# Kernel tuning notes

Measured on AMD Instinct MI355X. Metric: run time of the kernel, lower is better.

Reference implementation:

```python
import jax, jax.numpy as jnp
import numpy as np

# fixed seed frame used by rotate_matrix (same as torch init_matrix)
INIT_MATRIX = jnp.array([[-np.sqrt(0.5), np.sqrt(1.5), 0.0],
                         [-np.sqrt(2.0), 0.0, 0.0],
                         [0.0, 0.0, 0.0]], dtype=jnp.float32)

N_ATOMS = 3_000_000  # 1M residues * 3 backbone atoms
FN = 3000            # number of fragments; L = N_ATOMS // FN = 1000


def setup_inputs() -> dict:
    key = jax.random.key(0)
    k1, k2, k3 = jax.random.split(key, 3)
    # realistic internal coordinates: bond lengths ~1.33-1.53A, angles ~1.9-2.1 rad,
    # dihedrals uniform in [-pi, pi]
    bond_length = 1.33 + 0.2 * jax.random.uniform(k1, (N_ATOMS,), dtype=jnp.float32)
    bond_angle = 1.9 + 0.2 * jax.random.uniform(k2, (N_ATOMS,), dtype=jnp.float32)
    dhd = (2.0 * jax.random.uniform(k3, (N_ATOMS,), dtype=jnp.float32) - 1.0) * np.float32(np.pi)
    inner_tensor = jnp.stack([bond_length, bond_angle, dhd], axis=1)  # [N,3]
    # non-collinear initial frame (first 3 mainchain atoms)
    mainchain_coord_tensor = jnp.array([[0.0, 0.0, 0.0],
                                        [1.46, 0.0, 0.0],
                                        [2.0, 1.4, 0.0]], dtype=jnp.float32)
    return {"inner_tensor": inner_tensor, "fn": FN,
            "mainchain_coord_tensor": mainchain_coord_tensor}


def _frame_rows(A, B, C):
    # rows [bc, cross(n,bc), n]; torch builds M = rows^T and does M @ p,
    # which equals p @ rows
    bc = C - B
    bc = bc / jnp.linalg.norm(bc)
    n = jnp.cross(B - A, bc)
    n = n / jnp.linalg.norm(n)
    return jnp.stack([bc, jnp.cross(n, bc), n])  # [3,3]


def _extend_fragment(local_pts):
    # sequential NeRF extension in the fragment-local frame (rotate_matrix)
    def step(carry, p):
        A, B, C = carry
        D = p @ _frame_rows(A, B, C) + C
        return (B, C, D), D
    init = (INIT_MATRIX[0], INIT_MATRIX[1], INIT_MATRIX[2])
    _, pts = jax.lax.scan(step, init, local_pts)
    return pts  # [L,3]


def reference(inner_tensor, fn, mainchain_coord_tensor):
    N = inner_tensor.shape[0]
    L = N // fn
    bond_length = inner_tensor[:, 0]
    bond_angle = inner_tensor[:, 1]
    dhd = inner_tensor[:, 2]
    # psi/omiga/phy re-interleave (identity permutation when N % 3 == 0)
    dhd_v = jnp.stack([dhd[0::3], dhd[1::3], dhd[2::3]], axis=1).reshape(N)
    r_cos = bond_length * jnp.cos(bond_angle)
    r_sin = bond_length * jnp.sin(bond_angle)
    point = jnp.stack([r_cos, jnp.cos(dhd_v) * r_sin, jnp.sin(dhd_v) * r_sin], axis=1)  # [N,3]
    # independent local fragment builds (vmapped over fragments)
    local = jax.vmap(_extend_fragment)(point.reshape(fn, L, 3))  # [fn,L,3]
    frame0 = mainchain_coord_tensor[:3]
    # sequential placement of fragments into global frame (srf2f)
    def place(frame, loc):
        A, B, C = frame[0], frame[1], frame[2]
        g = loc @ _frame_rows(A, B, C) + C  # [L,3]
        return g[-3:], g
    _, glob = jax.lax.scan(place, frame0, local)  # [fn,L,3]
    return jnp.concatenate([frame0, glob.reshape(fn * L, 3)], axis=0)  # [3+N,3]
```

## Files before the change

kernel.cpp:

```cpp
#include <hip/hip_runtime.h>

#define NSTEPS 25
#define SUBF   (NSTEPS * 3)
#define BLK    256

struct Xf { float m[12]; };

__device__ __forceinline__ Xf xf_identity() {
    Xf o;
    o.m[0]=1.f;o.m[1]=0.f;o.m[2]=0.f;
    o.m[3]=0.f;o.m[4]=1.f;o.m[5]=0.f;
    o.m[6]=0.f;o.m[7]=0.f;o.m[8]=1.f;
    o.m[9]=0.f;o.m[10]=0.f;o.m[11]=0.f;
    return o;
}

__device__ __forceinline__ Xf xf_compose(const Xf& a, const Xf& b) {
    Xf o;
#pragma unroll
    for (int i = 0; i < 3; ++i)
#pragma unroll
        for (int c = 0; c < 3; ++c)
            o.m[i*3+c] = b.m[i*3+0]*a.m[0+c] + b.m[i*3+1]*a.m[3+c] + b.m[i*3+2]*a.m[6+c];
#pragma unroll
    for (int c = 0; c < 3; ++c)
        o.m[9+c] = b.m[9+0]*a.m[0+c] + b.m[9+1]*a.m[3+c] + b.m[9+2]*a.m[6+c] + a.m[9+c];
    return o;
}

__device__ __forceinline__ void xf_store_g(float* p, const Xf& x) {
    float4* q = (float4*)p;
    q[0] = make_float4(x.m[0], x.m[1], x.m[2],  x.m[3]);
    q[1] = make_float4(x.m[4], x.m[5], x.m[6],  x.m[7]);
    q[2] = make_float4(x.m[8], x.m[9], x.m[10], x.m[11]);
}

__device__ __forceinline__ Xf xf_load_g(const float* p) {
    const float4* q = (const float4*)p;
    float4 a = q[0], b = q[1], c = q[2];
    Xf o;
    o.m[0]=a.x; o.m[1]=a.y; o.m[2]=a.z;  o.m[3]=a.w;
    o.m[4]=b.x; o.m[5]=b.y; o.m[6]=b.z;  o.m[7]=b.w;
    o.m[8]=c.x; o.m[9]=c.y; o.m[10]=c.z; o.m[11]=c.w;
    return o;
}

__device__ __forceinline__ Xf xf_shflup(const Xf& x, int d) {
    Xf o;
#pragma unroll
    for (int i = 0; i < 12; ++i) o.m[i] = __shfl_up(x.m[i], d, 64);
    return o;
}

__device__ __forceinline__ void nerf_step(float bl, float ba, float ph,
    float& upx, float& upy, float& upz,
    float& ux,  float& uy,  float& uz,
    float& cx,  float& cy,  float& cz) {
    float sb, cb, sp, cp;
    __sincosf(ba, &sb, &cb);
    __sincosf(ph, &sp, &cp);
    float px = bl * cb;
    float rs = bl * sb;
    float py = cp * rs;
    float pz = sp * rs;
    float nx = upy*uz - upz*uy;
    float ny = upz*ux - upx*uz;
    float nz = upx*uy - upy*ux;
    float rin = __builtin_amdgcn_rsqf(nx*nx + ny*ny + nz*nz);
    nx *= rin; ny *= rin; nz *= rin;
    float mx = ny*uz - nz*uy;
    float my = nz*ux - nx*uz;
    float mz = nx*uy - ny*ux;
    float dx = px*ux + py*mx + pz*nx;
    float dy = px*uy + py*my + pz*ny;
    float dz = px*uz + py*mz + pz*nz;
    cx += dx; cy += dy; cz += dz;
    float ribl = __builtin_amdgcn_rcpf(bl);
    upx = ux; upy = uy; upz = uz;
    ux = dx*ribl; uy = dy*ribl; uz = dz*ribl;
}

#define UP0X (-0.5f)
#define UP0Y (-0.86602540378443865f)

__device__ __forceinline__ Xf make_T0(const float* __restrict__ mc) {
    float Ax=mc[0], Ay=mc[1], Az=mc[2];
    float Bx=mc[3], By=mc[4], Bz=mc[5];
    float Cx=mc[6], Cy=mc[7], Cz=mc[8];
    float bx = Cx-Bx, by = Cy-By, bz = Cz-Bz;
    float rb = __builtin_amdgcn_rsqf(bx*bx + by*by + bz*bz);
    bx *= rb; by *= rb; bz *= rb;
    float ex = Bx-Ax, ey = By-Ay, ez = Bz-Az;
    float nx = ey*bz - ez*by;
    float ny = ez*bx - ex*bz;
    float nz = ex*by - ey*bx;
    float rn = __builtin_amdgcn_rsqf(nx*nx + ny*ny + nz*nz);
    nx *= rn; ny *= rn; nz *= rn;
    float mx = ny*bz - nz*by;
    float my = nz*bx - nx*bz;
    float mz = nx*by - ny*bx;
    Xf T0;
    T0.m[0]=bx; T0.m[1]=by; T0.m[2]=bz;
    T0.m[3]=mx; T0.m[4]=my; T0.m[5]=mz;
    T0.m[6]=nx; T0.m[7]=ny; T0.m[8]=nz;
    T0.m[9]=Cx; T0.m[10]=Cy; T0.m[11]=Cz;
    return T0;
}

__global__ void __launch_bounds__(BLK, 2) k_links(
    const float* __restrict__ inner, float* __restrict__ thrPre,
    float* __restrict__ blockLink, int nsub, int nfTot)
{
    __shared__ __align__(16) float data[BLK * SUBF];
    __shared__ float sc[4 * 12];

    const int tid  = threadIdx.x;
    const int lane = tid & 63;
    const int wv   = tid >> 6;
    const int bid  = blockIdx.x;
    const int j    = bid * BLK + tid;
    const long base_f = (long)bid * (BLK * SUBF);
    int nf = nfTot - (int)base_f;
    if (nf > BLK * SUBF) nf = BLK * SUBF;

    {
        const float4* src4 = (const float4*)(inner + base_f);
        float4* dst4 = (float4*)data;
        for (int i4 = tid; i4 < (BLK * SUBF) / 4; i4 += BLK)
            if (i4 * 4 < nf) dst4[i4] = src4[i4];
    }
    __syncthreads();

    Xf L = xf_identity();
    if (j < nsub) {
        float upx=UP0X, upy=UP0Y, upz=0.f;
        float ux=1.f, uy=0.f, uz=0.f;
        float cx=0.f, cy=0.f, cz=0.f;
        const float* src = data + tid * SUBF;
        for (int k = 0; k < NSTEPS; ++k)
            nerf_step(src[3*k], src[3*k+1], src[3*k+2],
                      upx,upy,upz, ux,uy,uz, cx,cy,cz);
        float nx = upy*uz - upz*uy;
        float ny = upz*ux - upx*uz;
        float nz = upx*uy - upy*ux;
        float rin = __builtin_amdgcn_rsqf(nx*nx + ny*ny + nz*nz);
        nx *= rin; ny *= rin; nz *= rin;
        float mx = ny*uz - nz*uy;
        float my = nz*ux - nx*uz;
        float mz = nx*uy - ny*ux;
        L.m[0]=ux; L.m[1]=uy; L.m[2]=uz;
        L.m[3]=mx; L.m[4]=my; L.m[5]=mz;
        L.m[6]=nx; L.m[7]=ny; L.m[8]=nz;
        L.m[9]=cx; L.m[10]=cy; L.m[11]=cz;
    }

    Xf incl = L;
#pragma unroll
    for (int d = 1; d < 64; d <<= 1) {
        Xf p = xf_shflup(incl, d);
        if (lane >= d) incl = xf_compose(p, incl);
    }
    Xf laneEx = xf_shflup(incl, 1);
    if (lane == 0) laneEx = xf_identity();

    if (lane == 63) {
#pragma unroll
        for (int i = 0; i < 12; ++i) sc[wv*12 + i] = incl.m[i];
    }
    __syncthreads();

    Xf waveEx = xf_identity();
    for (int w = 0; w < wv; ++w) {
        Xf s;
#pragma unroll
        for (int i = 0; i < 12; ++i) s.m[i] = sc[w*12 + i];
        waveEx = xf_compose(waveEx, s);
    }
    Xf thrEx = xf_compose(waveEx, laneEx);

    if (j < nsub) {
#pragma unroll
        for (int i = 0; i < 12; ++i) thrPre[(size_t)i * nsub + j] = thrEx.m[i];
    }
    if (tid == 0) {
        Xf bt;
#pragma unroll
        for (int i = 0; i < 12; ++i) bt.m[i] = sc[i];
        for (int w = 1; w < 4; ++w) {
            Xf s;
#pragma unroll
            for (int i = 0; i < 12; ++i) s.m[i] = sc[w*12 + i];
            bt = xf_compose(bt, s);
        }
        xf_store_g(blockLink + (size_t)bid * 12, bt);
    }
}

__global__ void __launch_bounds__(BLK) k_scan(
    const float* __restrict__ blockLink, const float* __restrict__ mc,
    float* __restrict__ blockPrefix, float* __restrict__ out, int NB)
{
    __shared__ float sc[4 * 12];
    const int tid  = threadIdx.x;
    const int lane = tid & 63;
    const int wv   = tid >> 6;

    int i0 = 2*tid, i1 = 2*tid + 1;
    Xf e0 = (i0 < NB) ? xf_load_g(blockLink + (size_t)i0*12) : xf_identity();
    Xf e1 = (i1 < NB) ? xf_load_g(blockLink + (size_t)i1*12) : xf_identity();
    Xf pin = xf_compose(e0, e1);

    Xf inc2 = pin;
#pragma unroll
    for (int d = 1; d < 64; d <<= 1) {
        Xf p = xf_shflup(inc2, d);
        if (lane >= d) inc2 = xf_compose(p, inc2);
    }
    Xf pl = xf_shflup(inc2, 1);
    if (lane == 0) pl = xf_identity();
    if (lane == 63) {
#pragma unroll
        for (int i = 0; i < 12; ++i) sc[wv*12 + i] = inc2.m[i];
    }
    __syncthreads();
    Xf wex = xf_identity();
    for (int w = 0; w < wv; ++w) {
        Xf s;
#pragma unroll
        for (int i = 0; i < 12; ++i) s.m[i] = sc[w*12 + i];
        wex = xf_compose(wex, s);
    }

    Xf T0 = make_T0(mc);
    Xf g0 = xf_compose(xf_compose(T0, wex), pl);
    Xf g1 = xf_compose(g0, e0);
    if (i0 < NB) xf_store_g(blockPrefix + (size_t)i0*12, g0);
    if (i1 < NB) xf_store_g(blockPrefix + (size_t)i1*12, g1);

    if (tid == 0) {
#pragma unroll
        for (int i = 0; i < 9; ++i) out[i] = mc[i];
    }
}

__global__ void __launch_bounds__(BLK, 2) k_emit(
    const float* __restrict__ inner, const float* __restrict__ thrPre,
    const float* __restrict__ blockPrefix, float* __restrict__ out,
    int nsub, int nfTot)
{
    __shared__ __align__(16) float data[BLK * SUBF];

    const int tid  = threadIdx.x;
    const int bid  = blockIdx.x;
    const int j    = bid * BLK + tid;
    const long base_f = (long)bid * (BLK * SUBF);
    int nf = nfTot - (int)base_f;
    if (nf > BLK * SUBF) nf = BLK * SUBF;

    {
        const float4* src4 = (const float4*)(inner + base_f);
        float4* dst4 = (float4*)data;
        for (int i4 = tid; i4 < (BLK * SUBF) / 4; i4 += BLK)
            if (i4 * 4 < nf) dst4[i4] = src4[i4];
    }
    __syncthreads();

    if (j < nsub) {
        Xf bp = xf_load_g(blockPrefix + (size_t)bid * 12);
        Xf te;
#pragma unroll
        for (int i = 0; i < 12; ++i) te.m[i] = thrPre[(size_t)i * nsub + j];
        Xf T = xf_compose(bp, te);

        float ux = T.m[0], uy = T.m[1], uz = T.m[2];
        float upx = UP0X*T.m[0] + UP0Y*T.m[3];
        float upy = UP0X*T.m[1] + UP0Y*T.m[4];
        float upz = UP0X*T.m[2] + UP0Y*T.m[5];
        float cx = T.m[9], cy = T.m[10], cz = T.m[11];
        float* s = data + tid * SUBF;
        for (int k = 0; k < NSTEPS; ++k) {
            float bl = s[3*k], ba = s[3*k+1], ph = s[3*k+2];
            nerf_step(bl, ba, ph, upx,upy,upz, ux,uy,uz, cx,cy,cz);
            s[3*k] = cx; s[3*k+1] = cy; s[3*k+2] = cz;
        }
    }
    __syncthreads();

    {
        float* dst = out + 9 + base_f;
        for (int i = tid; i < nf; i += BLK) dst[i] = data[i];
    }
}

extern "C" void kernel_launch(void* const* d_in, const int* in_sizes, int n_in,
                              void* d_out, int out_size, void* d_ws, size_t ws_size,
                              hipStream_t stream) {
    const float* inner = (const float*)d_in[0];
    const float* mc    = (const float*)d_in[2];
    float* out = (float*)d_out;

    int nfTot = in_sizes[0];
    int N     = nfTot / 3;
    int nsub  = N / NSTEPS;
    int NB    = (nsub + BLK - 1) / BLK;

    float* thrPre      = (float*)d_ws;
    float* blockLink   = thrPre + (size_t)12 * nsub;
    float* blockPrefix = blockLink + (size_t)NB * 12;

    k_links<<<NB, BLK, 0, stream>>>(inner, thrPre, blockLink, nsub, nfTot);
    k_scan<<<1, BLK, 0, stream>>>(blockLink, mc, blockPrefix, out, NB);
    k_emit<<<NB, BLK, 0, stream>>>(inner, thrPre, blockPrefix, out, nsub, nfTot);
}
```

Baseline: 44.16 us.

## Fuse three-pass scan into single kernel with decoupled lookback

Merges the link, block-scan and emit kernels into one kernel. Each block publishes its aggregate transform with a release flag, and wave 0 walks back over earlier blocks' flags to build the exclusive prefix. This removes the second read of the inputs, the per-thread prefix round trip through global memory and two launch boundaries. The cost is a memset launch and spin-waiting, whose correctness depends on blocks being scheduled in order, plus a lookback whose length grows linearly with block index.

```diff
diff --git a/kernel.cpp b/kernel.cpp
--- a/kernel.cpp
+++ b/kernel.cpp
@@ -107,12 +107,14 @@
     return T0;
 }
 
-__global__ void __launch_bounds__(BLK, 2) k_links(
-    const float* __restrict__ inner, float* __restrict__ thrPre,
-    float* __restrict__ blockLink, int nsub, int nfTot)
+__global__ void __launch_bounds__(BLK, 2) k_fused(
+    const float* __restrict__ inner, const float* __restrict__ mc,
+    float* __restrict__ out, float* __restrict__ links,
+    int* __restrict__ flags, int nsub, int NB, int nfTot)
 {
     __shared__ __align__(16) float data[BLK * SUBF];
     __shared__ float sc[4 * 12];
+    __shared__ float sbx[12];
 
     const int tid  = threadIdx.x;
     const int lane = tid & 63;
@@ -178,100 +180,57 @@
     }
     Xf thrEx = xf_compose(waveEx, laneEx);
 
-    if (j < nsub) {
-#pragma unroll
-        for (int i = 0; i < 12; ++i) thrPre[(size_t)i * nsub + j] = thrEx.m[i];
-    }
     if (tid == 0) {
-        Xf bt;
-#pragma unroll
-        for (int i = 0; i < 12; ++i) bt.m[i] = sc[i];
+        Xf agg;
+#pragma unroll
+        for (int i = 0; i < 12; ++i) agg.m[i] = sc[i];
         for (int w = 1; w < 4; ++w) {
             Xf s;
 #pragma unroll
             for (int i = 0; i < 12; ++i) s.m[i] = sc[w*12 + i];
-            bt = xf_compose(bt, s);
-        }
-        xf_store_g(blockLink + (size_t)bid * 12, bt);
-    }
-}
-
-__global__ void __launch_bounds__(BLK) k_scan(
-    const float* __restrict__ blockLink, const float* __restrict__ mc,
-    float* __restrict__ blockPrefix, float* __restrict__ out, int NB)
-{
-    __shared__ float sc[4 * 12];
-    const int tid  = threadIdx.x;
-    const int lane = tid & 63;
-    const int wv   = tid >> 6;
-
-    int i0 = 2*tid, i1 = 2*tid + 1;
-    Xf e0 = (i0 < NB) ? xf_load_g(blockLink + (size_t)i0*12) : xf_identity();
-    Xf e1 = (i1 < NB) ? xf_load_g(blockLink + (size_t)i1*12) : xf_identity();
-    Xf pin = xf_compose(e0, e1);
-
-    Xf inc2 = pin;
-#pragma unroll
-    for (int d = 1; d < 64; d <<= 1) {
-        Xf p = xf_shflup(inc2, d);
-        if (lane >= d) inc2 = xf_compose(p, inc2);
-    }
-    Xf pl = xf_shflup(inc2, 1);
-    if (lane == 0) pl = xf_identity();
-    if (lane == 63) {
-#pragma unroll
-        for (int i = 0; i < 12; ++i) sc[wv*12 + i] = inc2.m[i];
-    }
-    __syncthreads();
-    Xf wex = xf_identity();
-    for (int w = 0; w < wv; ++w) {
-        Xf s;
-#pragma unroll
-        for (int i = 0; i < 12; ++i) s.m[i] = sc[w*12 + i];
-        wex = xf_compose(wex, s);
-    }
-
-    Xf T0 = make_T0(mc);
-    Xf g0 = xf_compose(xf_compose(T0, wex), pl);
-    Xf g1 = xf_compose(g0, e0);
-    if (i0 < NB) xf_store_g(blockPrefix + (size_t)i0*12, g0);
-    if (i1 < NB) xf_store_g(blockPrefix + (size_t)i1*12, g1);
-
-    if (tid == 0) {
-#pragma unroll
-        for (int i = 0; i < 9; ++i) out[i] = mc[i];
-    }
-}
-
-__global__ void __launch_bounds__(BLK, 2) k_emit(
-    const float* __restrict__ inner, const float* __restrict__ thrPre,
-    const float* __restrict__ blockPrefix, float* __restrict__ out,
-    int nsub, int nfTot)
-{
-    __shared__ __align__(16) float data[BLK * SUBF];
-
-    const int tid  = threadIdx.x;
-    const int bid  = blockIdx.x;
-    const int j    = bid * BLK + tid;
-    const long base_f = (long)bid * (BLK * SUBF);
-    int nf = nfTot - (int)base_f;
-    if (nf > BLK * SUBF) nf = BLK * SUBF;
-
-    {
-        const float4* src4 = (const float4*)(inner + base_f);
-        float4* dst4 = (float4*)data;
-        for (int i4 = tid; i4 < (BLK * SUBF) / 4; i4 += BLK)
-            if (i4 * 4 < nf) dst4[i4] = src4[i4];
-    }
-    __syncthreads();
+            agg = xf_compose(agg, s);
+        }
+        xf_store_g(links + (size_t)bid * 12, agg);
+        __threadfence();
+        __hip_atomic_store(&flags[bid], 1, __ATOMIC_RELEASE, __HIP_MEMORY_SCOPE_AGENT);
+    }
+
+    if (wv == 0) {
+        Xf S = xf_identity();
+        for (int pos = bid - 1; pos >= 0; pos -= 64) {
+            int idx = pos - 63 + lane;
+            Xf E = xf_identity();
+            if (idx >= 0) {
+                while (__hip_atomic_load(&flags[idx], __ATOMIC_ACQUIRE,
+                                         __HIP_MEMORY_SCOPE_AGENT) == 0)
+                    __builtin_amdgcn_s_sleep(2);
+                E = xf_load_g(links + (size_t)idx * 12);
+            }
+            Xf inc = E;
+#pragma unroll
+            for (int d = 1; d < 64; d <<= 1) {
+                Xf p = xf_shflup(inc, d);
+                if (lane >= d) inc = xf_compose(p, inc);
+            }
+            Xf W;
+#pragma unroll
+            for (int i = 0; i < 12; ++i) W.m[i] = __shfl(inc.m[i], 63, 64);
+            S = xf_compose(W, S);
+        }
+        if (lane == 0) {
+#pragma unroll
+            for (int i = 0; i < 12; ++i) sbx[i] = S.m[i];
+        }
+    }
+    __syncthreads();
+
+    Xf blockEx;
+#pragma unroll
+    for (int i = 0; i < 12; ++i) blockEx.m[i] = sbx[i];
 
     if (j < nsub) {
-        Xf bp = xf_load_g(blockPrefix + (size_t)bid * 12);
-        Xf te;
-#pragma unroll
-        for (int i = 0; i < 12; ++i) te.m[i] = thrPre[(size_t)i * nsub + j];
-        Xf T = xf_compose(bp, te);
-
+        Xf T0 = make_T0(mc);
+        Xf T  = xf_compose(xf_compose(T0, blockEx), thrEx);
         float ux = T.m[0], uy = T.m[1], uz = T.m[2];
         float upx = UP0X*T.m[0] + UP0Y*T.m[3];
         float upy = UP0X*T.m[1] + UP0Y*T.m[4];
@@ -290,6 +249,10 @@
         float* dst = out + 9 + base_f;
         for (int i = tid; i < nf; i += BLK) dst[i] = data[i];
     }
+    if (bid == 0 && tid == 0) {
+#pragma unroll
+        for (int i = 0; i < 9; ++i) out[i] = mc[i];
+    }
 }
 
 extern "C" void kernel_launch(void* const* d_in, const int* in_sizes, int n_in,
@@ -304,11 +267,10 @@
     int nsub  = N / NSTEPS;
     int NB    = (nsub + BLK - 1) / BLK;
 
-    float* thrPre      = (float*)d_ws;
-    float* blockLink   = thrPre + (size_t)12 * nsub;
-    float* blockPrefix = blockLink + (size_t)NB * 12;
-
-    k_links<<<NB, BLK, 0, stream>>>(inner, thrPre, blockLink, nsub, nfTot);
-    k_scan<<<1, BLK, 0, stream>>>(blockLink, mc, blockPrefix, out, NB);
-    k_emit<<<NB, BLK, 0, stream>>>(inner, thrPre, blockPrefix, out, nsub, nfTot);
-}
+    float* links = (float*)d_ws;
+    int*   flags = (int*)(links + (size_t)NB * 12);
+
+    hipMemsetAsync(flags, 0, (size_t)NB * sizeof(int), stream);
+
+    k_fused<<<NB, BLK, 0, stream>>>(inner, mc, out, links, flags, nsub, NB, nfTot);
+}
```

Result: slower. 71.32 us (+61.5%).

## Store block-local points in pass one, apply block prefix transform in emit

Applied to the files above, without the earlier changes.

The first kernel now writes out each point after the NeRF recurrence, already transformed into block-local coordinates by the thread's exclusive prefix. The emit kernel then only applies one rigid transform per point instead of rerunning the 25-step recurrence with its trig and normalisations. This drops the second sequential pass and the per-thread prefix storage. In exchange it writes and rereads a full-size intermediate point buffer through global memory, and numerical error may differ because transforms are composed in a different order.

```diff
diff --git a/kernel.cpp b/kernel.cpp
--- a/kernel.cpp
+++ b/kernel.cpp
@@ -3,6 +3,7 @@
 #define NSTEPS 25
 #define SUBF   (NSTEPS * 3)
 #define BLK    256
+#define TILE_F (BLK * SUBF)
 
 struct Xf { float m[12]; };
 
@@ -108,10 +109,10 @@
 }
 
 __global__ void __launch_bounds__(BLK, 2) k_links(
-    const float* __restrict__ inner, float* __restrict__ thrPre,
-    float* __restrict__ blockLink, int nsub, int nfTot)
+    const float* __restrict__ inner, float* __restrict__ pts,
+    float* __restrict__ links, int nsub, int nfTot)
 {
-    __shared__ __align__(16) float data[BLK * SUBF];
+    __shared__ __align__(16) float data[TILE_F];
     __shared__ float sc[4 * 12];
 
     const int tid  = threadIdx.x;
@@ -119,14 +120,14 @@
     const int wv   = tid >> 6;
     const int bid  = blockIdx.x;
     const int j    = bid * BLK + tid;
-    const long base_f = (long)bid * (BLK * SUBF);
+    const long base_f = (long)bid * TILE_F;
     int nf = nfTot - (int)base_f;
-    if (nf > BLK * SUBF) nf = BLK * SUBF;
+    if (nf > TILE_F) nf = TILE_F;
 
     {
         const float4* src4 = (const float4*)(inner + base_f);
         float4* dst4 = (float4*)data;
-        for (int i4 = tid; i4 < (BLK * SUBF) / 4; i4 += BLK)
+        for (int i4 = tid; i4 < TILE_F / 4; i4 += BLK)
             if (i4 * 4 < nf) dst4[i4] = src4[i4];
     }
     __syncthreads();
@@ -136,10 +137,12 @@
         float upx=UP0X, upy=UP0Y, upz=0.f;
         float ux=1.f, uy=0.f, uz=0.f;
         float cx=0.f, cy=0.f, cz=0.f;
-        const float* src = data + tid * SUBF;
-        for (int k = 0; k < NSTEPS; ++k)
-            nerf_step(src[3*k], src[3*k+1], src[3*k+2],
-                      upx,upy,upz, ux,uy,uz, cx,cy,cz);
+        float* s = data + tid * SUBF;
+        for (int k = 0; k < NSTEPS; ++k) {
+            float bl = s[3*k], ba = s[3*k+1], ph = s[3*k+2];
+            nerf_step(bl, ba, ph, upx,upy,upz, ux,uy,uz, cx,cy,cz);
+            s[3*k] = cx; s[3*k+1] = cy; s[3*k+2] = cz;
+        }
         float nx = upy*uz - upz*uy;
         float ny = upz*ux - upx*uz;
         float nz = upx*uy - upy*ux;
@@ -179,25 +182,40 @@
     Xf thrEx = xf_compose(waveEx, laneEx);
 
     if (j < nsub) {
-#pragma unroll
-        for (int i = 0; i < 12; ++i) thrPre[(size_t)i * nsub + j] = thrEx.m[i];
-    }
+        float* s = data + tid * SUBF;
+#pragma unroll
+        for (int k = 0; k < NSTEPS; ++k) {
+            float px = s[3*k], py = s[3*k+1], pz = s[3*k+2];
+            s[3*k]   = px*thrEx.m[0] + py*thrEx.m[3] + pz*thrEx.m[6] + thrEx.m[9];
+            s[3*k+1] = px*thrEx.m[1] + py*thrEx.m[4] + pz*thrEx.m[7] + thrEx.m[10];
+            s[3*k+2] = px*thrEx.m[2] + py*thrEx.m[5] + pz*thrEx.m[8] + thrEx.m[11];
+        }
+    }
+
     if (tid == 0) {
-        Xf bt;
-#pragma unroll
-        for (int i = 0; i < 12; ++i) bt.m[i] = sc[i];
+        Xf agg;
+#pragma unroll
+        for (int i = 0; i < 12; ++i) agg.m[i] = sc[i];
         for (int w = 1; w < 4; ++w) {
             Xf s;
 #pragma unroll
             for (int i = 0; i < 12; ++i) s.m[i] = sc[w*12 + i];
-            bt = xf_compose(bt, s);
+            agg = xf_compose(agg, s);
         }
-        xf_store_g(blockLink + (size_t)bid * 12, bt);
+        xf_store_g(links + (size_t)bid * 12, agg);
+    }
+    __syncthreads();
+
+    {
+        const float4* src4 = (const float4*)data;
+        float4* dst4 = (float4*)(pts + base_f);
+        for (int i4 = tid; i4 < TILE_F / 4; i4 += BLK)
+            if (i4 * 4 < nf) dst4[i4] = src4[i4];
     }
 }
 
 __global__ void __launch_bounds__(BLK) k_scan(
-    const float* __restrict__ blockLink, const float* __restrict__ mc,
+    const float* __restrict__ links, const float* __restrict__ mc,
     float* __restrict__ blockPrefix, float* __restrict__ out, int NB)
 {
     __shared__ float sc[4 * 12];
@@ -206,8 +224,8 @@
     const int wv   = tid >> 6;
 
     int i0 = 2*tid, i1 = 2*tid + 1;
-    Xf e0 = (i0 < NB) ? xf_load_g(blockLink + (size_t)i0*12) : xf_identity();
-    Xf e1 = (i1 < NB) ? xf_load_g(blockLink + (size_t)i1*12) : xf_identity();
+    Xf e0 = (i0 < NB) ? xf_load_g(links + (size_t)i0*12) : xf_identity();
+    Xf e1 = (i1 < NB) ? xf_load_g(links + (size_t)i1*12) : xf_identity();
     Xf pin = xf_compose(e0, e1);
 
     Xf inc2 = pin;
@@ -244,51 +262,34 @@
 }
 
 __global__ void __launch_bounds__(BLK, 2) k_emit(
-    const float* __restrict__ inner, const float* __restrict__ thrPre,
-    const float* __restrict__ blockPrefix, float* __restrict__ out,
-    int nsub, int nfTot)
+    const float* __restrict__ pts, const float* __restrict__ blockPrefix,
+    float* __restrict__ out, int nfTot)
 {
-    __shared__ __align__(16) float data[BLK * SUBF];
+    __shared__ __align__(16) float data[TILE_F];
 
     const int tid  = threadIdx.x;
     const int bid  = blockIdx.x;
-    const int j    = bid * BLK + tid;
-    const long base_f = (long)bid * (BLK * SUBF);
+    const long base_f = (long)bid * TILE_F;
     int nf = nfTot - (int)base_f;
-    if (nf > BLK * SUBF) nf = BLK * SUBF;
+    if (nf > TILE_F) nf = TILE_F;
 
     {
-        const float4* src4 = (const float4*)(inner + base_f);
+        const float4* src4 = (const float4*)(pts + base_f);
         float4* dst4 = (float4*)data;
-        for (int i4 = tid; i4 < (BLK * SUBF) / 4; i4 += BLK)
+        for (int i4 = tid; i4 < TILE_F / 4; i4 += BLK)
             if (i4 * 4 < nf) dst4[i4] = src4[i4];
     }
-    __syncthreads();
-
-    if (j < nsub) {
-        Xf bp = xf_load_g(blockPrefix + (size_t)bid * 12);
-        Xf te;
-#pragma unroll
-        for (int i = 0; i < 12; ++i) te.m[i] = thrPre[(size_t)i * nsub + j];
-        Xf T = xf_compose(bp, te);
-
-        float ux = T.m[0], uy = T.m[1], uz = T.m[2];
-        float upx = UP0X*T.m[0] + UP0Y*T.m[3];
-        float upy = UP0X*T.m[1] + UP0Y*T.m[4];
-        float upz = UP0X*T.m[2] + UP0Y*T.m[5];
-        float cx = T.m[9], cy = T.m[10], cz = T.m[11];
-        float* s = data + tid * SUBF;
-        for (int k = 0; k < NSTEPS; ++k) {
-            float bl = s[3*k], ba = s[3*k+1], ph = s[3*k+2];
-            nerf_step(bl, ba, ph, upx,upy,upz, ux,uy,uz, cx,cy,cz);
-            s[3*k] = cx; s[3*k+1] = cy; s[3*k+2] = cz;
-        }
-    }
+
+    Xf T = xf_load_g(blockPrefix + (size_t)bid * 12);
     __syncthreads();
 
     {
         float* dst = out + 9 + base_f;
-        for (int i = tid; i < nf; i += BLK) dst[i] = data[i];
+        for (int i = tid; i < nf; i += BLK) {
+            int p = i / 3, c = i - 3 * p;
+            float px = data[3*p], py = data[3*p+1], pz = data[3*p+2];
+            dst[i] = px*T.m[0+c] + py*T.m[3+c] + pz*T.m[6+c] + T.m[9+c];
+        }
     }
 }
 
@@ -304,11 +305,11 @@
     int nsub  = N / NSTEPS;
     int NB    = (nsub + BLK - 1) / BLK;
 
-    float* thrPre      = (float*)d_ws;
-    float* blockLink   = thrPre + (size_t)12 * nsub;
-    float* blockPrefix = blockLink + (size_t)NB * 12;
-
-    k_links<<<NB, BLK, 0, stream>>>(inner, thrPre, blockLink, nsub, nfTot);
-    k_scan<<<1, BLK, 0, stream>>>(blockLink, mc, blockPrefix, out, NB);
-    k_emit<<<NB, BLK, 0, stream>>>(inner, thrPre, blockPrefix, out, nsub, nfTot);
-}
+    float* pts         = (float*)d_ws;
+    float* links       = pts + (size_t)nfTot;
+    float* blockPrefix = links + (size_t)NB * 12;
+
+    k_links<<<NB, BLK, 0, stream>>>(inner, pts, links, nsub, nfTot);
+    k_scan<<<1, BLK, 0, stream>>>(links, mc, blockPrefix, out, NB);
+    k_emit<<<NB, BLK, 0, stream>>>(pts, blockPrefix, out, nfTot);
+}
```

Result: slower. 67.62 us (+53.1%).

## Process two sub-fragments per thread to add ILP and halve scan width

Applied to the files above, without the earlier changes.

Each thread now runs two independent NeRF chains interleaved, with blocks of 128 threads covering 256 sub-fragments. The pair is composed before the wave scan, which halves the shuffle-scan work and reduces the cross-wave combine to two waves. The goal is more instruction-level parallelism in the latency-bound sequential steps. In exchange there are fewer waves per block, more registers per thread and a changed thrPre layout. An odd nsub would leave the last sub-fragment without a stored prefix.

```diff
diff --git a/kernel.cpp b/kernel.cpp
--- a/kernel.cpp
+++ b/kernel.cpp
@@ -2,7 +2,9 @@
 
 #define NSTEPS 25
 #define SUBF   (NSTEPS * 3)
-#define BLK    256
+#define BLK    128
+#define PAIRS  (BLK * 2)
+#define TILE_F (PAIRS * SUBF)
 
 struct Xf { float m[12]; };
 
@@ -83,6 +85,26 @@
 #define UP0X (-0.5f)
 #define UP0Y (-0.86602540378443865f)
 
+__device__ __forceinline__ Xf link_from_state(
+    float upx, float upy, float upz,
+    float ux,  float uy,  float uz,
+    float cx,  float cy,  float cz) {
+    float nx = upy*uz - upz*uy;
+    float ny = upz*ux - upx*uz;
+    float nz = upx*uy - upy*ux;
+    float rin = __builtin_amdgcn_rsqf(nx*nx + ny*ny + nz*nz);
+    nx *= rin; ny *= rin; nz *= rin;
+    float mx = ny*uz - nz*uy;
+    float my = nz*ux - nx*uz;
+    float mz = nx*uy - ny*ux;
+    Xf L;
+    L.m[0]=ux; L.m[1]=uy; L.m[2]=uz;
+    L.m[3]=mx; L.m[4]=my; L.m[5]=mz;
+    L.m[6]=nx; L.m[7]=ny; L.m[8]=nz;
+    L.m[9]=cx; L.m[10]=cy; L.m[11]=cz;
+    return L;
+}
+
 __device__ __forceinline__ Xf make_T0(const float* __restrict__ mc) {
     float Ax=mc[0], Ay=mc[1], Az=mc[2];
     float Bx=mc[3], By=mc[4], Bz=mc[5];
@@ -107,58 +129,52 @@
     return T0;
 }
 
-__global__ void __launch_bounds__(BLK, 2) k_links(
+__global__ void __launch_bounds__(BLK, 1) k_links(
     const float* __restrict__ inner, float* __restrict__ thrPre,
     float* __restrict__ blockLink, int nsub, int nfTot)
 {
-    __shared__ __align__(16) float data[BLK * SUBF];
-    __shared__ float sc[4 * 12];
+    __shared__ __align__(16) float data[TILE_F];
+    __shared__ float sc[2 * 12];
 
     const int tid  = threadIdx.x;
     const int lane = tid & 63;
     const int wv   = tid >> 6;
     const int bid  = blockIdx.x;
-    const int j    = bid * BLK + tid;
-    const long base_f = (long)bid * (BLK * SUBF);
+    const int jp   = bid * PAIRS + 2 * tid;
+    const int npair = nsub >> 1;
+    const int p    = bid * BLK + tid;
+    const long base_f = (long)bid * TILE_F;
     int nf = nfTot - (int)base_f;
-    if (nf > BLK * SUBF) nf = BLK * SUBF;
+    if (nf > TILE_F) nf = TILE_F;
 
     {
         const float4* src4 = (const float4*)(inner + base_f);
         float4* dst4 = (float4*)data;
-        for (int i4 = tid; i4 < (BLK * SUBF) / 4; i4 += BLK)
+        for (int i4 = tid; i4 < TILE_F / 4; i4 += BLK)
             if (i4 * 4 < nf) dst4[i4] = src4[i4];
     }
     __syncthreads();
 
-    Xf L = xf_identity();
-    if (j < nsub) {
-        float upx=UP0X, upy=UP0Y, upz=0.f;
-        float ux=1.f, uy=0.f, uz=0.f;
-        float cx=0.f, cy=0.f, cz=0.f;
-        const float* src = data + tid * SUBF;
-        for (int k = 0; k < NSTEPS; ++k)
-            nerf_step(src[3*k], src[3*k+1], src[3*k+2],
-                      upx,upy,upz, ux,uy,uz, cx,cy,cz);
-        float nx = upy*uz - upz*uy;
-        float ny = upz*ux - upx*uz;
-        float nz = upx*uy - upy*ux;
-        float rin = __builtin_amdgcn_rsqf(nx*nx + ny*ny + nz*nz);
-        nx *= rin; ny *= rin; nz *= rin;
-        float mx = ny*uz - nz*uy;
-        float my = nz*ux - nx*uz;
-        float mz = nx*uy - ny*ux;
-        L.m[0]=ux; L.m[1]=uy; L.m[2]=uz;
-        L.m[3]=mx; L.m[4]=my; L.m[5]=mz;
-        L.m[6]=nx; L.m[7]=ny; L.m[8]=nz;
-        L.m[9]=cx; L.m[10]=cy; L.m[11]=cz;
-    }
-
-    Xf incl = L;
+    const bool aA = (jp < nsub), aB = (jp + 1 < nsub);
+    float Aux=1.f, Auy=0.f, Auz=0.f, Aupx=UP0X, Aupy=UP0Y, Aupz=0.f, Acx=0.f, Acy=0.f, Acz=0.f;
+    float Bux=1.f, Buy=0.f, Buz=0.f, Bupx=UP0X, Bupy=UP0Y, Bupz=0.f, Bcx=0.f, Bcy=0.f, Bcz=0.f;
+    const float* sA = data + (2 * tid) * SUBF;
+    const float* sB = sA + SUBF;
+    for (int k = 0; k < NSTEPS; ++k) {
+        if (aA) nerf_step(sA[3*k], sA[3*k+1], sA[3*k+2],
+                          Aupx,Aupy,Aupz, Aux,Auy,Auz, Acx,Acy,Acz);
+        if (aB) nerf_step(sB[3*k], sB[3*k+1], sB[3*k+2],
+                          Bupx,Bupy,Bupz, Bux,Buy,Buz, Bcx,Bcy,Bcz);
+    }
+    Xf LA = aA ? link_from_state(Aupx,Aupy,Aupz, Aux,Auy,Auz, Acx,Acy,Acz) : xf_identity();
+    Xf LB = aB ? link_from_state(Bupx,Bupy,Bupz, Bux,Buy,Buz, Bcx,Bcy,Bcz) : xf_identity();
+    Xf P  = xf_compose(LA, LB);
+
+    Xf incl = P;
 #pragma unroll
     for (int d = 1; d < 64; d <<= 1) {
-        Xf p = xf_shflup(incl, d);
-        if (lane >= d) incl = xf_compose(p, incl);
+        Xf q = xf_shflup(incl, d);
+        if (lane >= d) incl = xf_compose(q, incl);
     }
     Xf laneEx = xf_shflup(incl, 1);
     if (lane == 0) laneEx = xf_identity();
@@ -169,34 +185,32 @@
     }
     __syncthreads();
 
-    Xf waveEx = xf_identity();
-    for (int w = 0; w < wv; ++w) {
-        Xf s;
-#pragma unroll
-        for (int i = 0; i < 12; ++i) s.m[i] = sc[w*12 + i];
-        waveEx = xf_compose(waveEx, s);
-    }
-    Xf thrEx = xf_compose(waveEx, laneEx);
-
-    if (j < nsub) {
-#pragma unroll
-        for (int i = 0; i < 12; ++i) thrPre[(size_t)i * nsub + j] = thrEx.m[i];
+    Xf thrEx = laneEx;
+    if (wv == 1) {
+        Xf s0;
+#pragma unroll
+        for (int i = 0; i < 12; ++i) s0.m[i] = sc[i];
+        thrEx = xf_compose(s0, laneEx);
+    }
+    Xf ExA = thrEx;
+    Xf ExB = xf_compose(thrEx, LA);
+
+    if (p < npair) {
+#pragma unroll
+        for (int i = 0; i < 12; ++i) {
+            thrPre[((size_t)(2*i+0)) * npair + p] = ExA.m[i];
+            thrPre[((size_t)(2*i+1)) * npair + p] = ExB.m[i];
+        }
     }
     if (tid == 0) {
-        Xf bt;
-#pragma unroll
-        for (int i = 0; i < 12; ++i) bt.m[i] = sc[i];
-        for (int w = 1; w < 4; ++w) {
-            Xf s;
-#pragma unroll
-            for (int i = 0; i < 12; ++i) s.m[i] = sc[w*12 + i];
-            bt = xf_compose(bt, s);
-        }
-        xf_store_g(blockLink + (size_t)bid * 12, bt);
-    }
-}
-
-__global__ void __launch_bounds__(BLK) k_scan(
+        Xf s0, s1;
+#pragma unroll
+        for (int i = 0; i < 12; ++i) { s0.m[i] = sc[i]; s1.m[i] = sc[12+i]; }
+        xf_store_g(blockLink + (size_t)bid * 12, xf_compose(s0, s1));
+    }
+}
+
+__global__ void __launch_bounds__(256) k_scan(
     const float* __restrict__ blockLink, const float* __restrict__ mc,
     float* __restrict__ blockPrefix, float* __restrict__ out, int NB)
 {
@@ -213,8 +227,8 @@
     Xf inc2 = pin;
 #pragma unroll
     for (int d = 1; d < 64; d <<= 1) {
-        Xf p = xf_shflup(inc2, d);
-        if (lane >= d) inc2 = xf_compose(p, inc2);
+        Xf q = xf_shflup(inc2, d);
+        if (lane >= d) inc2 = xf_compose(q, inc2);
     }
     Xf pl = xf_shflup(inc2, 1);
     if (lane == 0) pl = xf_identity();
@@ -243,45 +257,67 @@
     }
 }
 
-__global__ void __launch_bounds__(BLK, 2) k_emit(
+__global__ void __launch_bounds__(BLK, 1) k_emit(
     const float* __restrict__ inner, const float* __restrict__ thrPre,
     const float* __restrict__ blockPrefix, float* __restrict__ out,
     int nsub, int nfTot)
 {
-    __shared__ __align__(16) float data[BLK * SUBF];
+    __shared__ __align__(16) float data[TILE_F];
 
     const int tid  = threadIdx.x;
     const int bid  = blockIdx.x;
-    const int j    = bid * BLK + tid;
-    const long base_f = (long)bid * (BLK * SUBF);
+    const int jp   = bid * PAIRS + 2 * tid;
+    const int npair = nsub >> 1;
+    const int p    = bid * BLK + tid;
+    const long base_f = (long)bid * TILE_F;
     int nf = nfTot - (int)base_f;
-    if (nf > BLK * SUBF) nf = BLK * SUBF;
+    if (nf > TILE_F) nf = TILE_F;
 
     {
         const float4* src4 = (const float4*)(inner + base_f);
         float4* dst4 = (float4*)data;
-        for (int i4 = tid; i4 < (BLK * SUBF) / 4; i4 += BLK)
+        for (int i4 = tid; i4 < TILE_F / 4; i4 += BLK)
             if (i4 * 4 < nf) dst4[i4] = src4[i4];
     }
     __syncthreads();
 
-    if (j < nsub) {
+    const bool aA = (jp < nsub), aB = (jp + 1 < nsub);
+    if (p < npair) {
         Xf bp = xf_load_g(blockPrefix + (size_t)bid * 12);
-        Xf te;
-#pragma unroll
-        for (int i = 0; i < 12; ++i) te.m[i] = thrPre[(size_t)i * nsub + j];
-        Xf T = xf_compose(bp, te);
-
-        float ux = T.m[0], uy = T.m[1], uz = T.m[2];
-        float upx = UP0X*T.m[0] + UP0Y*T.m[3];
-        float upy = UP0X*T.m[1] + UP0Y*T.m[4];
-        float upz = UP0X*T.m[2] + UP0Y*T.m[5];
-        float cx = T.m[9], cy = T.m[10], cz = T.m[11];
-        float* s = data + tid * SUBF;
+        Xf teA, teB;
+#pragma unroll
+        for (int i = 0; i < 12; ++i) {
+            teA.m[i] = thrPre[((size_t)(2*i+0)) * npair + p];
+            teB.m[i] = thrPre[((size_t)(2*i+1)) * npair + p];
+        }
+        Xf TA = xf_compose(bp, teA);
+        Xf TB = xf_compose(bp, teB);
+
+        float Aux = TA.m[0], Auy = TA.m[1], Auz = TA.m[2];
+        float Aupx = UP0X*TA.m[0] + UP0Y*TA.m[3];
+        float Aupy = UP0X*TA.m[1] + UP0Y*TA.m[4];
+        float Aupz = UP0X*TA.m[2] + UP0Y*TA.m[5];
+        float Acx = TA.m[9], Acy = TA.m[10], Acz = TA.m[11];
+
+        float Bux = TB.m[0], Buy = TB.m[1], Buz = TB.m[2];
+        float Bupx = UP0X*TB.m[0] + UP0Y*TB.m[3];
+        float Bupy = UP0X*TB.m[1] + UP0Y*TB.m[4];
+        float Bupz = UP0X*TB.m[2] + UP0Y*TB.m[5];
+        float Bcx = TB.m[9], Bcy = TB.m[10], Bcz = TB.m[11];
+
+        float* sA = data + (2 * tid) * SUBF;
+        float* sB = sA + SUBF;
         for (int k = 0; k < NSTEPS; ++k) {
-            float bl = s[3*k], ba = s[3*k+1], ph = s[3*k+2];
-            nerf_step(bl, ba, ph, upx,upy,upz, ux,uy,uz, cx,cy,cz);
-            s[3*k] = cx; s[3*k+1] = cy; s[3*k+2] = cz;
+            if (aA) {
+                float bl = sA[3*k], ba = sA[3*k+1], ph = sA[3*k+2];
+                nerf_step(bl, ba, ph, Aupx,Aupy,Aupz, Aux,Auy,Auz, Acx,Acy,Acz);
+                sA[3*k] = Acx; sA[3*k+1] = Acy; sA[3*k+2] = Acz;
+            }
+            if (aB) {
+                float bl = sB[3*k], ba = sB[3*k+1], ph = sB[3*k+2];
+                nerf_step(bl, ba, ph, Bupx,Bupy,Bupz, Bux,Buy,Buz, Bcx,Bcy,Bcz);
+                sB[3*k] = Bcx; sB[3*k+1] = Bcy; sB[3*k+2] = Bcz;
+            }
         }
     }
     __syncthreads();
@@ -302,13 +338,13 @@
     int nfTot = in_sizes[0];
     int N     = nfTot / 3;
     int nsub  = N / NSTEPS;
-    int NB    = (nsub + BLK - 1) / BLK;
+    int NB    = (nsub + PAIRS - 1) / PAIRS;
 
     float* thrPre      = (float*)d_ws;
     float* blockLink   = thrPre + (size_t)12 * nsub;
     float* blockPrefix = blockLink + (size_t)NB * 12;
 
     k_links<<<NB, BLK, 0, stream>>>(inner, thrPre, blockLink, nsub, nfTot);
-    k_scan<<<1, BLK, 0, stream>>>(blockLink, mc, blockPrefix, out, NB);
+    k_scan<<<1, 256, 0, stream>>>(blockLink, mc, blockPrefix, out, NB);
     k_emit<<<NB, BLK, 0, stream>>>(inner, thrPre, blockPrefix, out, nsub, nfTot);
 }
```

After: 59.43 us. +34.6%, slower.
